# Kernel tuning notes

Measured on AMD Instinct MI355X. Metric: run time of the kernel, lower is better.

The kernel has to match this reference:

```python
import jax, jax.numpy as jnp
import numpy as np

N_INST = 8      # number of instance labels present in target (== len(torch.unique(gt)))
DELTA_V = 0.5
ALPHA = 1.0
CLAMP_MAX = 100000.0


def setup_inputs() -> dict:
    key = jax.random.key(0)
    k1, k2 = jax.random.split(key)
    prediction = jax.random.normal(k1, (4, 16, 512, 512), dtype=jnp.float32)
    target = jax.random.randint(k2, (4, 512, 512), 0, N_INST)  # all labels 0..7 present whp
    return {"prediction": prediction, "target": target}


def _loss(prediction, target):
    B, nf, H, W = prediction.shape
    N = H * W
    pred = prediction.reshape(B, nf, N)                    # [B, nf, N]
    gt = target.reshape(B, N)                              # [B, N]
    # one-hot instance masks (unique sorted labels == arange(N_INST) by construction)
    mask = (gt[:, :, None] == jnp.arange(N_INST)[None, None, :]).astype(pred.dtype)  # [B, N, C]
    counts = mask.sum(axis=1)                              # [B, C] pixels per instance
    # per-instance means: sum of masked embeddings / counts
    means = jnp.einsum('bfn,bnc->bfc', pred, mask) / counts[:, None, :]  # [B, nf, C]
    # mu_expand - pred_masked = mask * (mu - pred); norm over feature dim
    diff = (means[:, :, None, :] - pred[:, :, :, None]) * mask[:, None, :, :]  # [B, nf, N, C]
    sq = jnp.sum(diff * diff, axis=1)                      # [B, N, C]
    # safe sqrt (zero where diff==0, matching torch.norm subgradient)
    d = jnp.where(sq > 0, jnp.sqrt(jnp.where(sq > 0, sq, 1.0)), 0.0)
    dist = jnp.clip(d - DELTA_V, 0.0, CLAMP_MAX) ** 2      # [B, N, C]
    # faithful to source: torch.sum(distance) is a full scalar reduce, then / counts, sum, / C
    l_var = dist.sum(axis=(1, 2)) * (1.0 / counts).sum(axis=1) / N_INST  # [B]
    return ALPHA * jnp.sum(l_var)


def reference(prediction, target):
    return _loss(prediction, target)
```

## Files before the change

kernel.cpp:

```cpp
#include <hip/hip_runtime.h>

#define NF   16
#define C    8
#define NB   4
#define NPIX (512*512)

#define SG      128
#define SCHUNK  (NPIX / SG)
#define SITERS  (SCHUNK / (64 * 4))

#define DG      128
#define DCHUNK  (NPIX / DG)
#define DITERS  (DCHUNK / (256 * 4))

#define WS_PSUM 0
#define WS_PCNT (NB * SG * 128)
#define WS_MEAN (WS_PCNT + NB * SG * 8)
#define WS_INV  (WS_MEAN + NB * 128)
#define WS_POUT (WS_INV + NB)

__global__ __launch_bounds__(256) void sums_kernel(const float* __restrict__ pred,
                                                   const int* __restrict__ tgt,
                                                   float* __restrict__ ws) {
    const int tid  = threadIdx.x;
    const int lane = tid & 63;
    const int wave = tid >> 6;
    const int b    = blockIdx.y;
    const int f0   = wave * 4;

    const float* predb = pred + (size_t)b * NF * NPIX;
    const int*   tgtb  = tgt  + (size_t)b * NPIX;
    const int start = blockIdx.x * SCHUNK;

    float acc[4][8];
#pragma unroll
    for (int i = 0; i < 4; ++i)
#pragma unroll
        for (int c = 0; c < 8; ++c) acc[i][c] = 0.0f;
    float cnt[8];
#pragma unroll
    for (int c = 0; c < 8; ++c) cnt[c] = 0.0f;

#pragma unroll 2
    for (int it = 0; it < SITERS; ++it) {
        const int base = start + it * 256 + lane * 4;
        int4 lab = *(const int4*)(tgtb + base);
        float4 p[4];
#pragma unroll
        for (int fi = 0; fi < 4; ++fi)
            p[fi] = *(const float4*)(predb + (f0 + fi) * NPIX + base);

        const int labs[4] = { lab.x, lab.y, lab.z, lab.w };
#pragma unroll
        for (int px = 0; px < 4; ++px) {
            const int lv = labs[px];
            float m[8];
#pragma unroll
            for (int c = 0; c < 8; ++c) m[c] = (lv == c) ? 1.0f : 0.0f;
            if (wave == 0) {
#pragma unroll
                for (int c = 0; c < 8; ++c) cnt[c] += m[c];
            }
#pragma unroll
            for (int fi = 0; fi < 4; ++fi) {
                const float pv = (px == 0) ? p[fi].x :
                                 (px == 1) ? p[fi].y :
                                 (px == 2) ? p[fi].z : p[fi].w;
#pragma unroll
                for (int c = 0; c < 8; ++c) acc[fi][c] += m[c] * pv;
            }
        }
    }

#pragma unroll
    for (int off = 32; off > 0; off >>= 1) {
#pragma unroll
        for (int fi = 0; fi < 4; ++fi)
#pragma unroll
            for (int c = 0; c < 8; ++c)
                acc[fi][c] += __shfl_xor(acc[fi][c], off);
    }
    if (wave == 0) {
#pragma unroll
        for (int off = 32; off > 0; off >>= 1)
#pragma unroll
            for (int c = 0; c < 8; ++c)
                cnt[c] += __shfl_xor(cnt[c], off);
    }

    {
        float v = 0.0f;
#pragma unroll
        for (int fj = 0; fj < 4; ++fj)
#pragma unroll
            for (int cj = 0; cj < 8; ++cj)
                v = (lane == fj * 8 + cj) ? acc[fj][cj] : v;
        if (lane < 32)
            ws[WS_PSUM + ((size_t)(b * SG + blockIdx.x)) * 128 + f0 * 8 + lane] = v;
        if (wave == 0) {
            float cv = 0.0f;
#pragma unroll
            for (int cj = 0; cj < 8; ++cj)
                cv = (lane == 32 + cj) ? cnt[cj] : cv;
            if (lane >= 32 && lane < 40)
                ws[WS_PCNT + (b * SG + blockIdx.x) * 8 + (lane - 32)] = cv;
        }
    }
}

__global__ void means_kernel(float* __restrict__ ws) {
    __shared__ float scnt[32];
    const int t = threadIdx.x;
    if (t < 32) {
        const int b = t >> 3, c = t & 7;
        float s = 0.0f;
        for (int blk = 0; blk < SG; ++blk)
            s += ws[WS_PCNT + (b * SG + blk) * 8 + c];
        scnt[t] = s;
    }
    __syncthreads();
    const int b = t >> 7, fc = t & 127, c = fc & 7;
    float s = 0.0f;
    for (int blk = 0; blk < SG; ++blk)
        s += ws[WS_PSUM + ((size_t)(b * SG + blk)) * 128 + fc];
    ws[WS_MEAN + b * 128 + fc] = s / scnt[b * 8 + c];
    if (fc == 0) {
        float iv = 0.0f;
#pragma unroll
        for (int c8 = 0; c8 < 8; ++c8) iv += 1.0f / scnt[b * 8 + c8];
        ws[WS_INV + b] = iv;
    }
}

__global__ __launch_bounds__(256) void dist_kernel(const float* __restrict__ pred,
                                                   const int* __restrict__ tgt,
                                                   const float* __restrict__ ws,
                                                   float* __restrict__ pout) {
    __shared__ float s_means[C * NF];
    __shared__ float s_red[4];
    const int tid = threadIdx.x;
    const int b   = blockIdx.y;
    if (tid < C * NF) s_means[tid] = ws[WS_MEAN + b * 128 + tid];
    const float invs = ws[WS_INV + b];
    __syncthreads();

    const float* predb = pred + (size_t)b * NF * NPIX;
    const int*   tgtb  = tgt  + (size_t)b * NPIX;

    float acc = 0.0f;
#pragma unroll
    for (int it = 0; it < DITERS; ++it) {
        const int base = blockIdx.x * DCHUNK + it * 1024 + tid * 4;
        int4 lab = *(const int4*)(tgtb + base);
        float s0 = 0.f, s1 = 0.f, s2 = 0.f, s3 = 0.f;
#pragma unroll
        for (int f = 0; f < NF; ++f) {
            float4 p = *(const float4*)(predb + f * NPIX + base);
            float d0 = s_means[f * C + lab.x] - p.x;
            float d1 = s_means[f * C + lab.y] - p.y;
            float d2 = s_means[f * C + lab.z] - p.z;
            float d3 = s_means[f * C + lab.w] - p.w;
            s0 += d0 * d0; s1 += d1 * d1; s2 += d2 * d2; s3 += d3 * d3;
        }
        float t0 = fminf(fmaxf(sqrtf(s0) - 0.5f, 0.0f), 100000.0f);
        float t1 = fminf(fmaxf(sqrtf(s1) - 0.5f, 0.0f), 100000.0f);
        float t2 = fminf(fmaxf(sqrtf(s2) - 0.5f, 0.0f), 100000.0f);
        float t3 = fminf(fmaxf(sqrtf(s3) - 0.5f, 0.0f), 100000.0f);
        acc += t0 * t0 + t1 * t1 + t2 * t2 + t3 * t3;
    }
#pragma unroll
    for (int off = 32; off > 0; off >>= 1) acc += __shfl_down(acc, off);
    const int lane = tid & 63, wave = tid >> 6;
    if (lane == 0) s_red[wave] = acc;
    __syncthreads();
    if (tid == 0) {
        float tot = s_red[0] + s_red[1] + s_red[2] + s_red[3];
        pout[b * DG + blockIdx.x] = tot * invs * 0.125f;
    }
}

__global__ void final_kernel(const float* __restrict__ pout, float* __restrict__ out) {
    __shared__ float sr[8];
    const int t = threadIdx.x;
    float v = pout[t];
#pragma unroll
    for (int off = 32; off > 0; off >>= 1) v += __shfl_xor(v, off);
    if ((t & 63) == 0) sr[t >> 6] = v;
    __syncthreads();
    if (t == 0) {
        float s = 0.0f;
#pragma unroll
        for (int i = 0; i < 8; ++i) s += sr[i];
        out[0] = s;
    }
}

extern "C" void kernel_launch(void* const* d_in, const int* in_sizes, int n_in,
                              void* d_out, int out_size, void* d_ws, size_t ws_size,
                              hipStream_t stream) {
    const float* pred = (const float*)d_in[0];
    const int*   tgt  = (const int*)d_in[1];
    float* out = (float*)d_out;
    float* ws  = (float*)d_ws;

    sums_kernel<<<dim3(SG, NB), dim3(256), 0, stream>>>(pred, tgt, ws);
    means_kernel<<<dim3(1), dim3(512), 0, stream>>>(ws);
    dist_kernel<<<dim3(DG, NB), dim3(256), 0, stream>>>(pred, tgt, ws, ws + WS_POUT);
    final_kernel<<<dim3(1), dim3(512), 0, stream>>>(ws + WS_POUT, out);
}
```

Before: 119.0 us.

## Double grid size and parallelize means reduction across blocks

Doubles the block count of the sums and dist kernels so each block handles half as many pixels, and fully unrolls the sums loop. The dist kernel now does a single iteration per thread. The means kernel is split across 8x4 blocks with a two-level shared-memory reduction, replacing one serial 512-thread block. The final reduction reads two partials per thread to match the larger partial array. The intent is more parallelism and occupancy on a large-CU GPU, at the cost of more partial sums to reduce.

```diff
diff --git a/kernel.cpp b/kernel.cpp
--- a/kernel.cpp
+++ b/kernel.cpp
@@ -5,13 +5,12 @@
 #define NB   4
 #define NPIX (512*512)
 
-#define SG      128
+#define SG      256
 #define SCHUNK  (NPIX / SG)
 #define SITERS  (SCHUNK / (64 * 4))
 
-#define DG      128
+#define DG      256
 #define DCHUNK  (NPIX / DG)
-#define DITERS  (DCHUNK / (256 * 4))
 
 #define WS_PSUM 0
 #define WS_PCNT (NB * SG * 128)
@@ -41,7 +40,7 @@
 #pragma unroll
     for (int c = 0; c < 8; ++c) cnt[c] = 0.0f;
 
-#pragma unroll 2
+#pragma unroll
     for (int it = 0; it < SITERS; ++it) {
         const int base = start + it * 256 + lane * 4;
         int4 lab = *(const int4*)(tgtb + base);
@@ -109,25 +108,47 @@
 }
 
 __global__ void means_kernel(float* __restrict__ ws) {
-    __shared__ float scnt[32];
-    const int t = threadIdx.x;
-    if (t < 32) {
-        const int b = t >> 3, c = t & 7;
-        float s = 0.0f;
-        for (int blk = 0; blk < SG; ++blk)
-            s += ws[WS_PCNT + (b * SG + blk) * 8 + c];
+    __shared__ float scnt_p[32 * 8];
+    __shared__ float scnt[8];
+    __shared__ float smean[16 * 16];
+    const int t = threadIdx.x, g = blockIdx.x, b = blockIdx.y;
+
+    {
+        const int c = t & 7, part = t >> 3;
+        float s = 0.0f;
+#pragma unroll
+        for (int i = 0; i < 8; ++i)
+            s += ws[WS_PCNT + (b * SG + part * 8 + i) * 8 + c];
+        scnt_p[part * 8 + c] = s;
+    }
+    __syncthreads();
+    if (t < 8) {
+        float s = 0.0f;
+        for (int p = 0; p < 32; ++p) s += scnt_p[p * 8 + t];
         scnt[t] = s;
     }
     __syncthreads();
-    const int b = t >> 7, fc = t & 127, c = fc & 7;
-    float s = 0.0f;
-    for (int blk = 0; blk < SG; ++blk)
-        s += ws[WS_PSUM + ((size_t)(b * SG + blk)) * 128 + fc];
-    ws[WS_MEAN + b * 128 + fc] = s / scnt[b * 8 + c];
-    if (fc == 0) {
+
+    {
+        const int fcl = t & 15, part = t >> 4;
+        const int fc = g * 16 + fcl;
+        float s = 0.0f;
+#pragma unroll
+        for (int i = 0; i < 16; ++i)
+            s += ws[WS_PSUM + (size_t)(b * SG + part * 16 + i) * 128 + fc];
+        smean[part * 16 + fcl] = s;
+    }
+    __syncthreads();
+    if (t < 16) {
+        float s = 0.0f;
+        for (int p = 0; p < 16; ++p) s += smean[p * 16 + t];
+        const int fc = g * 16 + t;
+        ws[WS_MEAN + b * 128 + fc] = s / scnt[fc & 7];
+    }
+    if (g == 0 && t == 0) {
         float iv = 0.0f;
 #pragma unroll
-        for (int c8 = 0; c8 < 8; ++c8) iv += 1.0f / scnt[b * 8 + c8];
+        for (int c = 0; c < 8; ++c) iv += 1.0f / scnt[c];
         ws[WS_INV + b] = iv;
     }
 }
@@ -147,27 +168,24 @@
     const float* predb = pred + (size_t)b * NF * NPIX;
     const int*   tgtb  = tgt  + (size_t)b * NPIX;
 
-    float acc = 0.0f;
-#pragma unroll
-    for (int it = 0; it < DITERS; ++it) {
-        const int base = blockIdx.x * DCHUNK + it * 1024 + tid * 4;
-        int4 lab = *(const int4*)(tgtb + base);
-        float s0 = 0.f, s1 = 0.f, s2 = 0.f, s3 = 0.f;
-#pragma unroll
-        for (int f = 0; f < NF; ++f) {
-            float4 p = *(const float4*)(predb + f * NPIX + base);
-            float d0 = s_means[f * C + lab.x] - p.x;
-            float d1 = s_means[f * C + lab.y] - p.y;
-            float d2 = s_means[f * C + lab.z] - p.z;
-            float d3 = s_means[f * C + lab.w] - p.w;
-            s0 += d0 * d0; s1 += d1 * d1; s2 += d2 * d2; s3 += d3 * d3;
-        }
-        float t0 = fminf(fmaxf(sqrtf(s0) - 0.5f, 0.0f), 100000.0f);
-        float t1 = fminf(fmaxf(sqrtf(s1) - 0.5f, 0.0f), 100000.0f);
-        float t2 = fminf(fmaxf(sqrtf(s2) - 0.5f, 0.0f), 100000.0f);
-        float t3 = fminf(fmaxf(sqrtf(s3) - 0.5f, 0.0f), 100000.0f);
-        acc += t0 * t0 + t1 * t1 + t2 * t2 + t3 * t3;
-    }
+    const int base = blockIdx.x * DCHUNK + tid * 4;
+    int4 lab = *(const int4*)(tgtb + base);
+    float s0 = 0.f, s1 = 0.f, s2 = 0.f, s3 = 0.f;
+#pragma unroll
+    for (int f = 0; f < NF; ++f) {
+        float4 p = *(const float4*)(predb + f * NPIX + base);
+        float d0 = s_means[f * C + lab.x] - p.x;
+        float d1 = s_means[f * C + lab.y] - p.y;
+        float d2 = s_means[f * C + lab.z] - p.z;
+        float d3 = s_means[f * C + lab.w] - p.w;
+        s0 += d0 * d0; s1 += d1 * d1; s2 += d2 * d2; s3 += d3 * d3;
+    }
+    float t0 = fminf(fmaxf(sqrtf(s0) - 0.5f, 0.0f), 100000.0f);
+    float t1 = fminf(fmaxf(sqrtf(s1) - 0.5f, 0.0f), 100000.0f);
+    float t2 = fminf(fmaxf(sqrtf(s2) - 0.5f, 0.0f), 100000.0f);
+    float t3 = fminf(fmaxf(sqrtf(s3) - 0.5f, 0.0f), 100000.0f);
+    float acc = t0 * t0 + t1 * t1 + t2 * t2 + t3 * t3;
+
 #pragma unroll
     for (int off = 32; off > 0; off >>= 1) acc += __shfl_down(acc, off);
     const int lane = tid & 63, wave = tid >> 6;
@@ -182,7 +200,7 @@
 __global__ void final_kernel(const float* __restrict__ pout, float* __restrict__ out) {
     __shared__ float sr[8];
     const int t = threadIdx.x;
-    float v = pout[t];
+    float v = pout[t] + pout[t + 512];
 #pragma unroll
     for (int off = 32; off > 0; off >>= 1) v += __shfl_xor(v, off);
     if ((t & 63) == 0) sr[t >> 6] = v;
@@ -204,7 +222,7 @@
     float* ws  = (float*)d_ws;
 
     sums_kernel<<<dim3(SG, NB), dim3(256), 0, stream>>>(pred, tgt, ws);
-    means_kernel<<<dim3(1), dim3(512), 0, stream>>>(ws);
+    means_kernel<<<dim3(8, NB), dim3(256), 0, stream>>>(ws);
     dist_kernel<<<dim3(DG, NB), dim3(256), 0, stream>>>(pred, tgt, ws, ws + WS_POUT);
     final_kernel<<<dim3(1), dim3(512), 0, stream>>>(ws + WS_POUT, out);
 }
```

After: 116.7 us. About the same (-1.9%).

## Fuse four kernels into one cooperative kernel with grid syncs

Applied to the files above, without the earlier changes.

Replaces the sums, means, dist and final kernels with a single cooperative kernel that uses grid-wide syncs between phases. Each block recomputes its batch's means redundantly from the partial sums rather than relying on a separate means kernel, and the same block handles the same pixel chunk in both passes. The aim is to remove launch gaps and possibly get L2 reuse of the prediction chunk between passes. In exchange it adds grid-sync cost, redundant per-block mean reductions, and needs all 512 blocks to be co-resident.

```diff
diff --git a/kernel.cpp b/kernel.cpp
--- a/kernel.cpp
+++ b/kernel.cpp
@@ -1,36 +1,45 @@
 #include <hip/hip_runtime.h>
+#include <hip/hip_cooperative_groups.h>
+
+namespace cg = cooperative_groups;
 
 #define NF   16
 #define C    8
 #define NB   4
 #define NPIX (512*512)
 
-#define SG      128
-#define SCHUNK  (NPIX / SG)
+#define NBLK    512
+#define BPB     128
+#define SCHUNK  (NPIX / BPB)
 #define SITERS  (SCHUNK / (64 * 4))
-
-#define DG      128
-#define DCHUNK  (NPIX / DG)
-#define DITERS  (DCHUNK / (256 * 4))
+#define DITERS  (SCHUNK / (256 * 4))
 
 #define WS_PSUM 0
-#define WS_PCNT (NB * SG * 128)
-#define WS_MEAN (WS_PCNT + NB * SG * 8)
-#define WS_INV  (WS_MEAN + NB * 128)
-#define WS_POUT (WS_INV + NB)
-
-__global__ __launch_bounds__(256) void sums_kernel(const float* __restrict__ pred,
-                                                   const int* __restrict__ tgt,
-                                                   float* __restrict__ ws) {
+#define WS_PCNT (NB * BPB * 128)
+#define WS_POUT (WS_PCNT + NB * BPB * 8)
+
+__global__ __launch_bounds__(256) void fused_kernel(const float* __restrict__ pred,
+                                                    const int* __restrict__ tgt,
+                                                    float* __restrict__ ws,
+                                                    float* __restrict__ out) {
     const int tid  = threadIdx.x;
     const int lane = tid & 63;
     const int wave = tid >> 6;
-    const int b    = blockIdx.y;
+    const int g    = blockIdx.x;
+    const int b    = g >> 7;
+    const int blk  = g & (BPB - 1);
     const int f0   = wave * 4;
 
     const float* predb = pred + (size_t)b * NF * NPIX;
     const int*   tgtb  = tgt  + (size_t)b * NPIX;
-    const int start = blockIdx.x * SCHUNK;
+    const int start = blk * SCHUNK;
+
+    __shared__ float smean_p[2][128];
+    __shared__ float scnt_p[8][8];
+    __shared__ float scnt[8];
+    __shared__ float s_mean[128];
+    __shared__ float s_invs;
+    __shared__ float s_red[4];
 
     float acc[4][8];
 #pragma unroll
@@ -96,102 +105,92 @@
             for (int cj = 0; cj < 8; ++cj)
                 v = (lane == fj * 8 + cj) ? acc[fj][cj] : v;
         if (lane < 32)
-            ws[WS_PSUM + ((size_t)(b * SG + blockIdx.x)) * 128 + f0 * 8 + lane] = v;
+            ws[WS_PSUM + ((size_t)(b * BPB + blk)) * 128 + f0 * 8 + lane] = v;
         if (wave == 0) {
             float cv = 0.0f;
 #pragma unroll
             for (int cj = 0; cj < 8; ++cj)
                 cv = (lane == 32 + cj) ? cnt[cj] : cv;
             if (lane >= 32 && lane < 40)
-                ws[WS_PCNT + (b * SG + blockIdx.x) * 8 + (lane - 32)] = cv;
+                ws[WS_PCNT + (b * BPB + blk) * 8 + (lane - 32)] = cv;
         }
     }
-}
-
-__global__ void means_kernel(float* __restrict__ ws) {
-    __shared__ float scnt[32];
-    const int t = threadIdx.x;
-    if (t < 32) {
-        const int b = t >> 3, c = t & 7;
+
+    cg::this_grid().sync();
+
+    if (tid < 64) {
+        const int c = tid & 7, grp = tid >> 3;
         float s = 0.0f;
-        for (int blk = 0; blk < SG; ++blk)
-            s += ws[WS_PCNT + (b * SG + blk) * 8 + c];
-        scnt[t] = s;
-    }
-    __syncthreads();
-    const int b = t >> 7, fc = t & 127, c = fc & 7;
-    float s = 0.0f;
-    for (int blk = 0; blk < SG; ++blk)
-        s += ws[WS_PSUM + ((size_t)(b * SG + blk)) * 128 + fc];
-    ws[WS_MEAN + b * 128 + fc] = s / scnt[b * 8 + c];
-    if (fc == 0) {
+#pragma unroll
+        for (int i = 0; i < 16; ++i)
+            s += ws[WS_PCNT + (b * BPB + grp * 16 + i) * 8 + c];
+        scnt_p[grp][c] = s;
+    }
+    {
+        const int fc = tid & 127, half = tid >> 7;
+        float s = 0.0f;
+        for (int i = 0; i < 64; ++i)
+            s += ws[WS_PSUM + ((size_t)(b * BPB + half * 64 + i)) * 128 + fc];
+        smean_p[half][fc] = s;
+    }
+    __syncthreads();
+    if (tid < 8) {
+        float s = 0.0f;
+#pragma unroll
+        for (int grp = 0; grp < 8; ++grp) s += scnt_p[grp][tid];
+        scnt[tid] = s;
+    }
+    __syncthreads();
+    if (tid < 128)
+        s_mean[tid] = (smean_p[0][tid] + smean_p[1][tid]) / scnt[tid & 7];
+    if (tid == 0) {
         float iv = 0.0f;
 #pragma unroll
-        for (int c8 = 0; c8 < 8; ++c8) iv += 1.0f / scnt[b * 8 + c8];
-        ws[WS_INV + b] = iv;
-    }
-}
-
-__global__ __launch_bounds__(256) void dist_kernel(const float* __restrict__ pred,
-                                                   const int* __restrict__ tgt,
-                                                   const float* __restrict__ ws,
-                                                   float* __restrict__ pout) {
-    __shared__ float s_means[C * NF];
-    __shared__ float s_red[4];
-    const int tid = threadIdx.x;
-    const int b   = blockIdx.y;
-    if (tid < C * NF) s_means[tid] = ws[WS_MEAN + b * 128 + tid];
-    const float invs = ws[WS_INV + b];
-    __syncthreads();
-
-    const float* predb = pred + (size_t)b * NF * NPIX;
-    const int*   tgtb  = tgt  + (size_t)b * NPIX;
-
-    float acc = 0.0f;
+        for (int c = 0; c < 8; ++c) iv += 1.0f / scnt[c];
+        s_invs = iv;
+    }
+    __syncthreads();
+
+    float dacc = 0.0f;
 #pragma unroll
     for (int it = 0; it < DITERS; ++it) {
-        const int base = blockIdx.x * DCHUNK + it * 1024 + tid * 4;
+        const int base = start + it * 1024 + tid * 4;
         int4 lab = *(const int4*)(tgtb + base);
         float s0 = 0.f, s1 = 0.f, s2 = 0.f, s3 = 0.f;
 #pragma unroll
         for (int f = 0; f < NF; ++f) {
             float4 p = *(const float4*)(predb + f * NPIX + base);
-            float d0 = s_means[f * C + lab.x] - p.x;
-            float d1 = s_means[f * C + lab.y] - p.y;
-            float d2 = s_means[f * C + lab.z] - p.z;
-            float d3 = s_means[f * C + lab.w] - p.w;
+            float d0 = s_mean[f * C + lab.x] - p.x;
+            float d1 = s_mean[f * C + lab.y] - p.y;
+            float d2 = s_mean[f * C + lab.z] - p.z;
+            float d3 = s_mean[f * C + lab.w] - p.w;
             s0 += d0 * d0; s1 += d1 * d1; s2 += d2 * d2; s3 += d3 * d3;
         }
         float t0 = fminf(fmaxf(sqrtf(s0) - 0.5f, 0.0f), 100000.0f);
         float t1 = fminf(fmaxf(sqrtf(s1) - 0.5f, 0.0f), 100000.0f);
         float t2 = fminf(fmaxf(sqrtf(s2) - 0.5f, 0.0f), 100000.0f);
         float t3 = fminf(fmaxf(sqrtf(s3) - 0.5f, 0.0f), 100000.0f);
-        acc += t0 * t0 + t1 * t1 + t2 * t2 + t3 * t3;
-    }
-#pragma unroll
-    for (int off = 32; off > 0; off >>= 1) acc += __shfl_down(acc, off);
-    const int lane = tid & 63, wave = tid >> 6;
-    if (lane == 0) s_red[wave] = acc;
+        dacc += t0 * t0 + t1 * t1 + t2 * t2 + t3 * t3;
+    }
+#pragma unroll
+    for (int off = 32; off > 0; off >>= 1) dacc += __shfl_down(dacc, off);
+    if (lane == 0) s_red[wave] = dacc;
     __syncthreads();
     if (tid == 0) {
         float tot = s_red[0] + s_red[1] + s_red[2] + s_red[3];
-        pout[b * DG + blockIdx.x] = tot * invs * 0.125f;
-    }
-}
-
-__global__ void final_kernel(const float* __restrict__ pout, float* __restrict__ out) {
-    __shared__ float sr[8];
-    const int t = threadIdx.x;
-    float v = pout[t];
-#pragma unroll
-    for (int off = 32; off > 0; off >>= 1) v += __shfl_xor(v, off);
-    if ((t & 63) == 0) sr[t >> 6] = v;
-    __syncthreads();
-    if (t == 0) {
-        float s = 0.0f;
-#pragma unroll
-        for (int i = 0; i < 8; ++i) s += sr[i];
-        out[0] = s;
+        ws[WS_POUT + g] = tot * s_invs * 0.125f;
+    }
+
+    cg::this_grid().sync();
+
+    if (g == 0) {
+        float v = ws[WS_POUT + tid] + ws[WS_POUT + tid + 256];
+#pragma unroll
+        for (int off = 32; off > 0; off >>= 1) v += __shfl_xor(v, off);
+        if (lane == 0) s_red[wave] = v;
+        __syncthreads();
+        if (tid == 0)
+            out[0] = s_red[0] + s_red[1] + s_red[2] + s_red[3];
     }
 }
 
@@ -203,8 +202,7 @@
     float* out = (float*)d_out;
     float* ws  = (float*)d_ws;
 
-    sums_kernel<<<dim3(SG, NB), dim3(256), 0, stream>>>(pred, tgt, ws);
-    means_kernel<<<dim3(1), dim3(512), 0, stream>>>(ws);
-    dist_kernel<<<dim3(DG, NB), dim3(256), 0, stream>>>(pred, tgt, ws, ws + WS_POUT);
-    final_kernel<<<dim3(1), dim3(512), 0, stream>>>(ws + WS_POUT, out);
+    void* args[] = { (void*)&pred, (void*)&tgt, (void*)&ws, (void*)&out };
+    hipLaunchCooperativeKernel((const void*)fused_kernel, dim3(NBLK), dim3(256),
+                               args, 0, stream);
 }
```

New measurement: 213.8 us. 79.6% more time.

## Split sums kernel per feature and double dist grid to raise parallelism

Applied to the files above, without the earlier changes.

The sums kernel's work split changes from one block per pixel chunk covering all 16 features to one block per (chunk, feature, batch), 1024 blocks in total, each holding 8 accumulators instead of 32. The aim is to cut register pressure and give more blocks to spread across the GPU. The dist kernel now launches 256 blocks per batch, so each thread handles a single group of 4 pixels, and the means and final kernels are updated to match. The cost is that label data is reread 16 times, once per feature, and there are more partial results to reduce.

```diff
diff --git a/kernel.cpp b/kernel.cpp
--- a/kernel.cpp
+++ b/kernel.cpp
@@ -5,82 +5,67 @@
 #define NB   4
 #define NPIX (512*512)
 
-#define SG      128
-#define SCHUNK  (NPIX / SG)
-#define SITERS  (SCHUNK / (64 * 4))
+#define CH      16
+#define CPX     (NPIX / CH)
+#define SITERS  (CPX / (256 * 4))
 
-#define DG      128
+#define DG      256
 #define DCHUNK  (NPIX / DG)
-#define DITERS  (DCHUNK / (256 * 4))
 
 #define WS_PSUM 0
-#define WS_PCNT (NB * SG * 128)
-#define WS_MEAN (WS_PCNT + NB * SG * 8)
+#define WS_PCNT (NB * NF * CH * 8)
+#define WS_MEAN (WS_PCNT + NB * CH * 8)
 #define WS_INV  (WS_MEAN + NB * 128)
 #define WS_POUT (WS_INV + NB)
 
 __global__ __launch_bounds__(256) void sums_kernel(const float* __restrict__ pred,
                                                    const int* __restrict__ tgt,
                                                    float* __restrict__ ws) {
-    const int tid  = threadIdx.x;
-    const int lane = tid & 63;
-    const int wave = tid >> 6;
-    const int b    = blockIdx.y;
-    const int f0   = wave * 4;
+    const int t    = threadIdx.x;
+    const int lane = t & 63;
+    const int wave = t >> 6;
+    const int ch   = blockIdx.x;
+    const int f    = blockIdx.y;
+    const int b    = blockIdx.z;
 
-    const float* predb = pred + (size_t)b * NF * NPIX;
-    const int*   tgtb  = tgt  + (size_t)b * NPIX;
-    const int start = blockIdx.x * SCHUNK;
+    const float* pf = pred + ((size_t)b * NF + f) * NPIX + ch * CPX;
+    const int*   tg = tgt  + (size_t)b * NPIX + ch * CPX;
 
-    float acc[4][8];
+    float acc[8];
 #pragma unroll
-    for (int i = 0; i < 4; ++i)
-#pragma unroll
-        for (int c = 0; c < 8; ++c) acc[i][c] = 0.0f;
+    for (int c = 0; c < 8; ++c) acc[c] = 0.0f;
     float cnt[8];
 #pragma unroll
     for (int c = 0; c < 8; ++c) cnt[c] = 0.0f;
 
-#pragma unroll 2
     for (int it = 0; it < SITERS; ++it) {
-        const int base = start + it * 256 + lane * 4;
-        int4 lab = *(const int4*)(tgtb + base);
-        float4 p[4];
+        const int px = it * 1024 + t * 4;
+        int4   lab = *(const int4*)(tg + px);
+        float4 p   = *(const float4*)(pf + px);
+        float m0[8], m1[8], m2[8], m3[8];
 #pragma unroll
-        for (int fi = 0; fi < 4; ++fi)
-            p[fi] = *(const float4*)(predb + (f0 + fi) * NPIX + base);
-
-        const int labs[4] = { lab.x, lab.y, lab.z, lab.w };
+        for (int c = 0; c < 8; ++c) {
+            m0[c] = (lab.x == c) ? 1.0f : 0.0f;
+            m1[c] = (lab.y == c) ? 1.0f : 0.0f;
+            m2[c] = (lab.z == c) ? 1.0f : 0.0f;
+            m3[c] = (lab.w == c) ? 1.0f : 0.0f;
+        }
 #pragma unroll
-        for (int px = 0; px < 4; ++px) {
-            const int lv = labs[px];
-            float m[8];
+        for (int c = 0; c < 8; ++c)
+            acc[c] += m0[c] * p.x + m1[c] * p.y + m2[c] * p.z + m3[c] * p.w;
+        if (f == 0) {
 #pragma unroll
-            for (int c = 0; c < 8; ++c) m[c] = (lv == c) ? 1.0f : 0.0f;
-            if (wave == 0) {
-#pragma unroll
-                for (int c = 0; c < 8; ++c) cnt[c] += m[c];
-            }
-#pragma unroll
-            for (int fi = 0; fi < 4; ++fi) {
-                const float pv = (px == 0) ? p[fi].x :
-                                 (px == 1) ? p[fi].y :
-                                 (px == 2) ? p[fi].z : p[fi].w;
-#pragma unroll
-                for (int c = 0; c < 8; ++c) acc[fi][c] += m[c] * pv;
-            }
+            for (int c = 0; c < 8; ++c)
+                cnt[c] += m0[c] + m1[c] + m2[c] + m3[c];
         }
     }
 
 #pragma unroll
-    for (int off = 32; off > 0; off >>= 1) {
+    for (int off = 32; off > 0; off >>= 1)
 #pragma unroll
-        for (int fi = 0; fi < 4; ++fi)
-#pragma unroll
-            for (int c = 0; c < 8; ++c)
-                acc[fi][c] += __shfl_xor(acc[fi][c], off);
-    }
-    if (wave == 0) {
+        for (int c = 0; c < 8; ++c)
+            acc[c] += __shfl_xor(acc[c], off);
+    if (f == 0) {
 #pragma unroll
         for (int off = 32; off > 0; off >>= 1)
 #pragma unroll
@@ -88,23 +73,23 @@
                 cnt[c] += __shfl_xor(cnt[c], off);
     }
 
-    {
-        float v = 0.0f;
+    __shared__ float sred[4][8];
+    __shared__ float scred[4][8];
+    if (lane == 0) {
 #pragma unroll
-        for (int fj = 0; fj < 4; ++fj)
+        for (int c = 0; c < 8; ++c) sred[wave][c] = acc[c];
+        if (f == 0)
 #pragma unroll
-            for (int cj = 0; cj < 8; ++cj)
-                v = (lane == fj * 8 + cj) ? acc[fj][cj] : v;
-        if (lane < 32)
-            ws[WS_PSUM + ((size_t)(b * SG + blockIdx.x)) * 128 + f0 * 8 + lane] = v;
-        if (wave == 0) {
-            float cv = 0.0f;
-#pragma unroll
-            for (int cj = 0; cj < 8; ++cj)
-                cv = (lane == 32 + cj) ? cnt[cj] : cv;
-            if (lane >= 32 && lane < 40)
-                ws[WS_PCNT + (b * SG + blockIdx.x) * 8 + (lane - 32)] = cv;
-        }
+            for (int c = 0; c < 8; ++c) scred[wave][c] = cnt[c];
+    }
+    __syncthreads();
+    if (t < 8)
+        ws[WS_PSUM + (((size_t)b * NF + f) * CH + ch) * 8 + t] =
+            sred[0][t] + sred[1][t] + sred[2][t] + sred[3][t];
+    if (f == 0 && t >= 8 && t < 16) {
+        const int c = t - 8;
+        ws[WS_PCNT + (b * CH + ch) * 8 + c] =
+            scred[0][c] + scred[1][c] + scred[2][c] + scred[3][c];
     }
 }
 
@@ -114,15 +99,17 @@
     if (t < 32) {
         const int b = t >> 3, c = t & 7;
         float s = 0.0f;
-        for (int blk = 0; blk < SG; ++blk)
-            s += ws[WS_PCNT + (b * SG + blk) * 8 + c];
+#pragma unroll
+        for (int ch = 0; ch < CH; ++ch)
+            s += ws[WS_PCNT + (b * CH + ch) * 8 + c];
         scnt[t] = s;
     }
     __syncthreads();
-    const int b = t >> 7, fc = t & 127, c = fc & 7;
+    const int b = t >> 7, fc = t & 127, f = fc >> 3, c = fc & 7;
     float s = 0.0f;
-    for (int blk = 0; blk < SG; ++blk)
-        s += ws[WS_PSUM + ((size_t)(b * SG + blk)) * 128 + fc];
+#pragma unroll
+    for (int ch = 0; ch < CH; ++ch)
+        s += ws[WS_PSUM + (((size_t)b * NF + f) * CH + ch) * 8 + c];
     ws[WS_MEAN + b * 128 + fc] = s / scnt[b * 8 + c];
     if (fc == 0) {
         float iv = 0.0f;
@@ -147,27 +134,24 @@
     const float* predb = pred + (size_t)b * NF * NPIX;
     const int*   tgtb  = tgt  + (size_t)b * NPIX;
 
-    float acc = 0.0f;
+    const int base = blockIdx.x * DCHUNK + tid * 4;
+    int4 lab = *(const int4*)(tgtb + base);
+    float s0 = 0.f, s1 = 0.f, s2 = 0.f, s3 = 0.f;
 #pragma unroll
-    for (int it = 0; it < DITERS; ++it) {
-        const int base = blockIdx.x * DCHUNK + it * 1024 + tid * 4;
-        int4 lab = *(const int4*)(tgtb + base);
-        float s0 = 0.f, s1 = 0.f, s2 = 0.f, s3 = 0.f;
-#pragma unroll
-        for (int f = 0; f < NF; ++f) {
-            float4 p = *(const float4*)(predb + f * NPIX + base);
-            float d0 = s_means[f * C + lab.x] - p.x;
-            float d1 = s_means[f * C + lab.y] - p.y;
-            float d2 = s_means[f * C + lab.z] - p.z;
-            float d3 = s_means[f * C + lab.w] - p.w;
-            s0 += d0 * d0; s1 += d1 * d1; s2 += d2 * d2; s3 += d3 * d3;
-        }
-        float t0 = fminf(fmaxf(sqrtf(s0) - 0.5f, 0.0f), 100000.0f);
-        float t1 = fminf(fmaxf(sqrtf(s1) - 0.5f, 0.0f), 100000.0f);
-        float t2 = fminf(fmaxf(sqrtf(s2) - 0.5f, 0.0f), 100000.0f);
-        float t3 = fminf(fmaxf(sqrtf(s3) - 0.5f, 0.0f), 100000.0f);
-        acc += t0 * t0 + t1 * t1 + t2 * t2 + t3 * t3;
+    for (int f = 0; f < NF; ++f) {
+        float4 p = *(const float4*)(predb + f * NPIX + base);
+        float d0 = s_means[f * C + lab.x] - p.x;
+        float d1 = s_means[f * C + lab.y] - p.y;
+        float d2 = s_means[f * C + lab.z] - p.z;
+        float d3 = s_means[f * C + lab.w] - p.w;
+        s0 += d0 * d0; s1 += d1 * d1; s2 += d2 * d2; s3 += d3 * d3;
     }
+    float t0 = fminf(fmaxf(sqrtf(s0) - 0.5f, 0.0f), 100000.0f);
+    float t1 = fminf(fmaxf(sqrtf(s1) - 0.5f, 0.0f), 100000.0f);
+    float t2 = fminf(fmaxf(sqrtf(s2) - 0.5f, 0.0f), 100000.0f);
+    float t3 = fminf(fmaxf(sqrtf(s3) - 0.5f, 0.0f), 100000.0f);
+    float acc = t0 * t0 + t1 * t1 + t2 * t2 + t3 * t3;
+
 #pragma unroll
     for (int off = 32; off > 0; off >>= 1) acc += __shfl_down(acc, off);
     const int lane = tid & 63, wave = tid >> 6;
@@ -182,7 +166,7 @@
 __global__ void final_kernel(const float* __restrict__ pout, float* __restrict__ out) {
     __shared__ float sr[8];
     const int t = threadIdx.x;
-    float v = pout[t];
+    float v = pout[t] + pout[t + 512];
 #pragma unroll
     for (int off = 32; off > 0; off >>= 1) v += __shfl_xor(v, off);
     if ((t & 63) == 0) sr[t >> 6] = v;
@@ -203,7 +187,7 @@
     float* out = (float*)d_out;
     float* ws  = (float*)d_ws;
 
-    sums_kernel<<<dim3(SG, NB), dim3(256), 0, stream>>>(pred, tgt, ws);
+    sums_kernel<<<dim3(CH, NF, NB), dim3(256), 0, stream>>>(pred, tgt, ws);
     means_kernel<<<dim3(1), dim3(512), 0, stream>>>(ws);
     dist_kernel<<<dim3(DG, NB), dim3(256), 0, stream>>>(pred, tgt, ws, ws + WS_POUT);
     final_kernel<<<dim3(1), dim3(512), 0, stream>>>(ws + WS_POUT, out);
```

After: 119.0 us. No clear change (+0.0%).
